# Kernel tuning notes

Measured on AMD Instinct MI355X. Metric: run time of the kernel, lower is better.

Reference implementation:

```python
import jax, jax.numpy as jnp
import numpy as np

N_TOKENS = 1024
HIDDEN = 2048
N_EXPERTS = 16
MOE_INTER = 1024
TOP_K = 6
N_GROUP = 4
TOPK_GROUP = 2
N_SHARED = 2
ROUTED_SCALING = 2.5
RENORM = True
CAPACITY = 1024  # >> N_TOKENS*TOP_K/N_EXPERTS = 384; overflow probability negligible


def setup_inputs() -> dict:
    key = jax.random.key(0)
    ks = jax.random.split(key, 7)
    s = 0.02
    return {
        'hidden_states': jax.random.normal(ks[0], (N_TOKENS, HIDDEN), jnp.float32),
        'gate_w': jax.random.normal(ks[1], (N_EXPERTS, HIDDEN), jnp.float32) * s,
        'gate_bias': jax.random.normal(ks[2], (N_EXPERTS,), jnp.float32) * s,
        'w_gate_up': jax.random.normal(ks[3], (N_EXPERTS, HIDDEN, 2 * MOE_INTER), jnp.float32) * s,
        'w_down': jax.random.normal(ks[4], (N_EXPERTS, MOE_INTER, HIDDEN), jnp.float32) * s,
        'shared_w_gate_up': jax.random.normal(ks[5], (HIDDEN, 2 * N_SHARED * MOE_INTER), jnp.float32) * s,
        'shared_w_down': jax.random.normal(ks[6], (N_SHARED * MOE_INTER, HIDDEN), jnp.float32) * s,
    }


def _swiglu(gu):
    # npu_swiglu with activate_left=True: silu(first half) * second half
    g, u = jnp.split(gu, 2, axis=-1)
    return jax.nn.silu(g) * u


def reference(hidden_states, gate_w, gate_bias, w_gate_up, w_down, shared_w_gate_up, shared_w_down):
    x = hidden_states
    N, H = x.shape
    E, K, C = N_EXPERTS, TOP_K, CAPACITY
    P = N * K  # number of (token, slot) pairs

    # ---- MoEGate: router logits + noaux_tc grouped top-k ----
    logits = x @ gate_w.T                              # [N, E]
    scores = jax.nn.sigmoid(logits)                    # sigmoid scoring (noaux_tc)
    s_corr = scores + gate_bias[None, :]
    sg = s_corr.reshape(N, N_GROUP, E // N_GROUP)
    group_scores = jax.lax.top_k(sg, 2)[0].sum(-1)     # top-2 sum per group [N, G]
    _, gidx = jax.lax.top_k(group_scores, TOPK_GROUP)
    gmask = jnp.sum(jax.nn.one_hot(gidx, N_GROUP, dtype=jnp.float32), axis=1) > 0
    masked = jnp.where(gmask[:, :, None], sg, -jnp.inf).reshape(N, E)
    _, topk_ids = jax.lax.top_k(masked, K)             # [N, K]
    w = jnp.take_along_axis(scores, topk_ids, axis=-1)  # weights from original scores
    if RENORM:
        w = w / jnp.sum(w, axis=-1, keepdims=True)
    w = w * ROUTED_SCALING

    # ---- dispatch: fixed-capacity buffers per expert ----
    flat_e = topk_ids.reshape(P)
    onehot = jax.nn.one_hot(flat_e, E, dtype=jnp.int32)
    pos = jnp.cumsum(onehot, axis=0)[jnp.arange(P), flat_e] - 1  # slot within expert
    valid = pos < C
    buf = jnp.full((E, C), P, jnp.int32).at[flat_e, jnp.clip(pos, 0, C - 1)].set(
        jnp.where(valid, jnp.arange(P, dtype=jnp.int32), P))
    tok = jnp.where(buf < P, buf // K, N)              # token index per slot, N = pad
    x_pad = jnp.concatenate([x, jnp.zeros((1, H), x.dtype)], axis=0)
    xe = x_pad[tok]                                    # [E, C, H]

    # ---- grouped expert GEMMs (SwiGLU MLP per expert) ----
    h = jnp.einsum('ech,ehi->eci', xe, w_gate_up)      # [E, C, 2I]
    y = jnp.einsum('eci,eih->ech', _swiglu(h), w_down)  # [E, C, H]

    # ---- combine: weighted scatter-add back to tokens ----
    w_pad = jnp.concatenate([w.reshape(P), jnp.zeros((1,), w.dtype)])
    pw = w_pad[jnp.where(buf < P, buf, P)]             # [E, C]
    routed = jnp.zeros((N + 1, H), x.dtype).at[tok].add(y * pw[:, :, None])[:N]

    # ---- shared experts (reduce_results=False, fused add) ----
    shared = _swiglu(x @ shared_w_gate_up) @ shared_w_down
    return routed + shared
```

## Files before the change

### kernel.cpp

```cpp
#include <hip/hip_runtime.h>
#include <hip/hip_bf16.h>
#include <math.h>

typedef __attribute__((ext_vector_type(8))) short bf16x8;
typedef __attribute__((ext_vector_type(4))) float f32x4;

#define N_TOK 1024
#define HID   2048
#define NEXP  16
#define NE2   18
#define INTER 1024
#define TOPK  6
#define CAP   1024

__device__ __forceinline__ unsigned short f2bf(float f) {
  unsigned u = __builtin_bit_cast(unsigned, f);
  u += 0x7fffu + ((u >> 16) & 1u);
  return (unsigned short)(u >> 16);
}
__device__ __forceinline__ float b2f(short s) {
  unsigned u = ((unsigned)(unsigned short)s) << 16;
  return __builtin_bit_cast(float, u);
}
__device__ __forceinline__ void gll16(const void* g, void* l) {
  __builtin_amdgcn_global_load_lds(
      (const __attribute__((address_space(1))) unsigned int*)g,
      (__attribute__((address_space(3))) unsigned int*)l, 16, 0, 0);
}

__global__ __launch_bounds__(256) void router_k(
    const float* __restrict__ x, const float* __restrict__ gw,
    const float* __restrict__ gb, int* __restrict__ counts,
    int* __restrict__ tok_list, int* __restrict__ meta,
    float* __restrict__ pwt, unsigned short* __restrict__ x_bf)
{
  const int t   = blockIdx.x;
  const int tid = threadIdx.x;
  __shared__ float xrow[HID];
  __shared__ float logits[NEXP];

  for (int i = tid; i < HID; i += 256) {
    float v = x[(size_t)t * HID + i];
    xrow[i] = v;
    x_bf[(size_t)t * HID + i] = f2bf(v);
  }
  __syncthreads();

  const int w = tid >> 6, lane = tid & 63;
  for (int s = 0; s < 4; ++s) {
    int e = w * 4 + s;
    const float* g = gw + (size_t)e * HID;
    float p = 0.f;
    for (int i = lane; i < HID; i += 64) p += xrow[i] * g[i];
    for (int off = 32; off; off >>= 1) p += __shfl_down(p, off);
    if (lane == 0) logits[e] = p;
  }
  __syncthreads();

  if (tid == 0) {
    float sc[NEXP], scorr[NEXP];
    for (int e = 0; e < NEXP; ++e) {
      float s1 = 1.f / (1.f + expf(-logits[e]));
      sc[e] = s1; scorr[e] = s1 + gb[e];
    }
    float gs[4];
    for (int g = 0; g < 4; ++g) {
      float m1 = -1e30f, m2 = -1e30f;
      for (int j = 0; j < 4; ++j) {
        float v = scorr[g * 4 + j];
        if (v > m1) { m2 = m1; m1 = v; } else if (v > m2) m2 = v;
      }
      gs[g] = m1 + m2;
    }
    int g1 = 0;
    for (int g = 1; g < 4; ++g) if (gs[g] > gs[g1]) g1 = g;
    int g2 = -1;
    for (int g = 0; g < 4; ++g) { if (g == g1) continue; if (g2 < 0 || gs[g] > gs[g2]) g2 = g; }

    bool taken[NEXP];
    for (int e = 0; e < NEXP; ++e) taken[e] = false;
    int ids[TOPK]; float wv[TOPK]; float wsum = 0.f;
    for (int k = 0; k < TOPK; ++k) {
      int best = -1; float bv = -1e30f;
      for (int e = 0; e < NEXP; ++e) {
        int grp = e >> 2;
        if (grp != g1 && grp != g2) continue;
        if (taken[e]) continue;
        if (scorr[e] > bv) { bv = scorr[e]; best = e; }
      }
      taken[best] = true; ids[k] = best; wv[k] = sc[best]; wsum += sc[best];
    }
    float inv = 2.5f / wsum;
    for (int k = 0; k < TOPK; ++k) {
      int e = ids[k];
      int slot = atomicAdd(&counts[e], 1);
      tok_list[e * CAP + slot] = t;
      meta[t * TOPK + k] = (e << 16) | slot;
      pwt[t * TOPK + k] = wv[k] * inv;
    }
  }
}

__global__ __launch_bounds__(256) void t_gu_k(
    const float* __restrict__ wgu, const float* __restrict__ sgu,
    unsigned short* __restrict__ dst)
{
  const int z = blockIdx.z;
  const int n0 = blockIdx.x * 64, k0 = blockIdx.y * 64;
  const float* src; int ld; int cb;
  if (z < 16) { src = wgu + (size_t)z * HID * (2 * INTER); ld = 2 * INTER; cb = n0; }
  else { int j = z - 16; src = sgu; ld = 4096;
         cb = (n0 < 1024) ? j * 1024 + n0 : 1024 * j + 1024 + n0; }
  __shared__ __align__(16) unsigned short t2[64][72];
  const int tid = threadIdx.x;
  const int kb = tid >> 4, nb = tid & 15;
  unsigned short h[4][4];
  #pragma unroll
  for (int j = 0; j < 4; ++j) {
    float4 f = *(const float4*)(src + (size_t)(k0 + kb * 4 + j) * ld + cb + nb * 4);
    h[j][0] = f2bf(f.x); h[j][1] = f2bf(f.y); h[j][2] = f2bf(f.z); h[j][3] = f2bf(f.w);
  }
  #pragma unroll
  for (int i = 0; i < 4; ++i) {
    int rr = nb * 4 + i;
    unsigned lo  = h[0][i] | ((unsigned)h[1][i] << 16);
    unsigned hi2 = h[2][i] | ((unsigned)h[3][i] << 16);
    unsigned long long v = (unsigned long long)lo | ((unsigned long long)hi2 << 32);
    *(unsigned long long*)((char*)t2 + rr * 144 + ((kb * 8) ^ ((rr & 7) << 4))) = v;
  }
  __syncthreads();
  unsigned short* d = dst + (size_t)z * HID * (2 * INTER);
  #pragma unroll
  for (int i = 0; i < 2; ++i) {
    int c = tid + 256 * i;
    int nl = c >> 3, s = c & 7;
    uint4 v = *(const uint4*)((const char*)t2 + nl * 144 + ((s * 16) ^ ((nl & 7) << 4)));
    *(uint4*)(d + (size_t)(n0 + nl) * HID + k0 + s * 8) = v;
  }
}

__global__ __launch_bounds__(256) void t_d_k(
    const float* __restrict__ wd, const float* __restrict__ sd,
    unsigned short* __restrict__ dst)
{
  const int z = blockIdx.z;
  const int n0 = blockIdx.x * 64, k0 = blockIdx.y * 64;
  const float* src = (z < 16) ? wd + (size_t)z * INTER * HID
                              : sd + (size_t)(z - 16) * INTER * HID;
  __shared__ __align__(16) unsigned short t2[64][72];
  const int tid = threadIdx.x;
  const int kb = tid >> 4, nb = tid & 15;
  unsigned short h[4][4];
  #pragma unroll
  for (int j = 0; j < 4; ++j) {
    float4 f = *(const float4*)(src + (size_t)(k0 + kb * 4 + j) * HID + n0 + nb * 4);
    h[j][0] = f2bf(f.x); h[j][1] = f2bf(f.y); h[j][2] = f2bf(f.z); h[j][3] = f2bf(f.w);
  }
  #pragma unroll
  for (int i = 0; i < 4; ++i) {
    int rr = nb * 4 + i;
    unsigned lo  = h[0][i] | ((unsigned)h[1][i] << 16);
    unsigned hi2 = h[2][i] | ((unsigned)h[3][i] << 16);
    unsigned long long v = (unsigned long long)lo | ((unsigned long long)hi2 << 32);
    *(unsigned long long*)((char*)t2 + rr * 144 + ((kb * 8) ^ ((rr & 7) << 4))) = v;
  }
  __syncthreads();
  unsigned short* d = dst + (size_t)z * HID * INTER;
  #pragma unroll
  for (int i = 0; i < 2; ++i) {
    int c = tid + 256 * i;
    int nl = c >> 3, s = c & 7;
    uint4 v = *(const uint4*)((const char*)t2 + nl * 144 + ((s * 16) ^ ((nl & 7) << 4)));
    *(uint4*)(d + (size_t)(n0 + nl) * INTER + k0 + s * 8) = v;
  }
}

template<int MODE>
__global__ __launch_bounds__(256, 2) void gemm_bf16_k(
    const unsigned short* __restrict__ A, int lda, size_t a_estride,
    const unsigned short* __restrict__ Wt, int K, size_t w_estride,
    const int* __restrict__ counts, const int* __restrict__ tok_list,
    unsigned short* __restrict__ outb, int out_ld, size_t out_estride)
{
  const int e  = blockIdx.z;
  const int m0 = blockIdx.y * 128;
  const int M  = (e < 16) ? counts[e] : N_TOK;
  if (m0 >= M) return;
  const int n0 = blockIdx.x * (MODE == 0 ? 128 : 256);

  __shared__ __align__(16) unsigned short Al[128 * 64];
  __shared__ __align__(16) unsigned short Bl[2][256 * 64];

  const int tid = threadIdx.x, lane = tid & 63, wid = tid >> 6;
  const int wm = wid >> 1, wn = wid & 1, l15 = lane & 15, hi = lane >> 4;

  const unsigned short* Ap = A + (size_t)e * a_estride;
  const unsigned short* Wp = Wt + (size_t)e * w_estride;

  const int r0 = tid >> 3, s0 = tid & 7, sl = s0 ^ (r0 & 7);
  const unsigned short* asrc[4]; int aoff[4];
  #pragma unroll
  for (int i = 0; i < 4; ++i) {
    int r = r0 + 32 * i;
    int slot = m0 + r;
    int row;
    if (MODE == 0) row = (e < 16) ? ((slot < M) ? tok_list[e * CAP + slot] : 0) : slot;
    else           row = slot;
    asrc[i] = Ap + (size_t)row * lda + sl * 8;
    aoff[i] = (tid + 256 * i) * 16;
  }
  const unsigned short* bpg;
  const unsigned short* bpu;
  if (MODE == 0) {
    bpg = Wp + (size_t)(n0 + r0) * K + sl * 8;
    bpu = Wp + (size_t)(1024 + n0 + r0) * K + sl * 8;
  } else {
    bpg = Wp + (size_t)(n0 + r0) * K + sl * 8;
    bpu = bpg + (size_t)128 * K;
  }
  const size_t bstep = (size_t)32 * K;

  int bn[8];
  #pragma unroll
  for (int ni = 0; ni < 8; ++ni) {
    if (MODE == 0) bn[ni] = (ni < 4) ? (wn * 64 + ni * 16) : (128 + wn * 64 + (ni - 4) * 16);
    else           bn[ni] = wn * 128 + ni * 16;
  }

  f32x4 acc[4][8];
  #pragma unroll
  for (int a0 = 0; a0 < 4; ++a0)
    #pragma unroll
    for (int b0 = 0; b0 < 8; ++b0) acc[a0][b0] = (f32x4){0.f, 0.f, 0.f, 0.f};

  #define ISSUE_B(buf, kt)                                                  \
    _Pragma("unroll")                                                       \
    for (int i = 0; i < 4; ++i)                                             \
      gll16(bpg + bstep * i + (kt), (char*)(buf) + (tid + 256 * i) * 16);   \
    _Pragma("unroll")                                                       \
    for (int i = 0; i < 4; ++i)                                             \
      gll16(bpu + bstep * i + (kt), (char*)(buf) + (tid + 256 * (i + 4)) * 16);
  #define ISSUE_A(kt)                                                       \
    _Pragma("unroll")                                                       \
    for (int i = 0; i < 4; ++i) gll16(asrc[i] + (kt), (char*)Al + aoff[i]);
  #define COMPUTE(Bb)                                                       \
    _Pragma("unroll")                                                       \
    for (int kk = 0; kk < 64; kk += 32) {                                   \
      bf16x8 af[4], bv[8];                                                  \
      _Pragma("unroll")                                                     \
      for (int mi = 0; mi < 4; ++mi) {                                      \
        int r = wm * 64 + mi * 16 + l15;                                    \
        int off = (r * 128 + (kk + hi * 8) * 2) ^ ((r & 7) << 4);           \
        af[mi] = *(const bf16x8*)((const char*)Al + off);                   \
      }                                                                     \
      _Pragma("unroll")                                                     \
      for (int ni = 0; ni < 8; ++ni) {                                      \
        int r = bn[ni] + l15;                                               \
        int off = (r * 128 + (kk + hi * 8) * 2) ^ ((r & 7) << 4);           \
        bv[ni] = *(const bf16x8*)((const char*)(Bb) + off);                 \
      }                                                                     \
      _Pragma("unroll")                                                     \
      for (int mi = 0; mi < 4; ++mi)                                        \
        _Pragma("unroll")                                                   \
        for (int ni = 0; ni < 8; ++ni)                                      \
          acc[mi][ni] = __builtin_amdgcn_mfma_f32_16x16x32_bf16(            \
              af[mi], bv[ni], acc[mi][ni], 0, 0, 0);                        \
    }

  const int nt = K >> 6;
  ISSUE_B(Bl[0], 0)
  ISSUE_A(0)
  asm volatile("s_waitcnt vmcnt(0)" ::: "memory");
  __builtin_amdgcn_s_barrier();

  int p = 0;
  for (int t = 0; t < nt; ++t) {
    const bool pf = (t + 1 < nt);
    if (pf) { ISSUE_B(Bl[p ^ 1], (t + 1) << 6) }
    COMPUTE(Bl[p])
    __builtin_amdgcn_s_barrier();
    if (pf) {
      ISSUE_A((t + 1) << 6)
      asm volatile("s_waitcnt vmcnt(0)" ::: "memory");
      __builtin_amdgcn_s_barrier();
    }
    p ^= 1;
  }
  #undef ISSUE_B
  #undef ISSUE_A
  #undef COMPUTE

  const int rbase = hi * 4;
  if (MODE == 0) {
    #pragma unroll
    for (int mi = 0; mi < 4; ++mi)
      #pragma unroll
      for (int rr = 0; rr < 4; ++rr) {
        int slot = m0 + wm * 64 + mi * 16 + rbase + rr;
        if (slot >= M) continue;
        #pragma unroll
        for (int ni = 0; ni < 4; ++ni) {
          float g = acc[mi][ni][rr], u = acc[mi][ni + 4][rr];
          float sv = g / (1.f + expf(-g)) * u;
          int col = n0 + wn * 64 + ni * 16 + l15;
          outb[(size_t)e * out_estride + (size_t)slot * out_ld + col] = f2bf(sv);
        }
      }
  } else {
    #pragma unroll
    for (int mi = 0; mi < 4; ++mi)
      #pragma unroll
      for (int rr = 0; rr < 4; ++rr) {
        int slot = m0 + wm * 64 + mi * 16 + rbase + rr;
        if (slot >= M) continue;
        unsigned short* row = outb + (size_t)e * out_estride + (size_t)slot * out_ld;
        #pragma unroll
        for (int ni = 0; ni < 8; ++ni)
          row[n0 + bn[ni] + l15] = f2bf(acc[mi][ni][rr]);
      }
  }
}

__global__ __launch_bounds__(256) void combine_k(
    const unsigned short* __restrict__ ybuf, const int* __restrict__ meta,
    const float* __restrict__ pwt, float* __restrict__ out)
{
  const int t = blockIdx.x;
  const int c0 = threadIdx.x * 8;
  float acc[8];
  {
    bf16x8 v0 = *(const bf16x8*)(ybuf + ((size_t)16 * CAP + t) * HID + c0);
    bf16x8 v1 = *(const bf16x8*)(ybuf + ((size_t)17 * CAP + t) * HID + c0);
    #pragma unroll
    for (int j = 0; j < 8; ++j) acc[j] = b2f(v0[j]) + b2f(v1[j]);
  }
  #pragma unroll
  for (int k = 0; k < TOPK; ++k) {
    int m = meta[t * TOPK + k];
    float w = pwt[t * TOPK + k];
    int e = m >> 16, s = m & 0xffff;
    bf16x8 v = *(const bf16x8*)(ybuf + ((size_t)e * CAP + s) * HID + c0);
    #pragma unroll
    for (int j = 0; j < 8; ++j) acc[j] += w * b2f(v[j]);
  }
  float4* o = (float4*)(out + (size_t)t * HID + c0);
  o[0] = make_float4(acc[0], acc[1], acc[2], acc[3]);
  o[1] = make_float4(acc[4], acc[5], acc[6], acc[7]);
}

extern "C" void kernel_launch(void* const* d_in, const int* in_sizes, int n_in,
                              void* d_out, int out_size, void* d_ws, size_t ws_size,
                              hipStream_t stream) {
  const float* x   = (const float*)d_in[0];
  const float* gw  = (const float*)d_in[1];
  const float* gb  = (const float*)d_in[2];
  const float* wgu = (const float*)d_in[3];
  const float* wd  = (const float*)d_in[4];
  const float* sgu = (const float*)d_in[5];
  const float* sd  = (const float*)d_in[6];
  float* out = (float*)d_out;

  char* ws = (char*)d_ws;
  int*   counts   = (int*)ws;
  int*   tok_list = (int*)(ws + 256);
  int*   meta     = (int*)(ws + 256 + 65536);
  float* pwt      = (float*)(ws + 256 + 65536 + 24576);
  unsigned short* x_bf  = (unsigned short*)(ws + 128 * 1024);
  unsigned short* act   = x_bf + (size_t)N_TOK * HID;
  unsigned short* ybuf  = act + (size_t)NE2 * CAP * INTER;
  unsigned short* wt_gu = ybuf + (size_t)NE2 * CAP * HID;
  unsigned short* wt_d  = wt_gu + (size_t)NE2 * HID * 2 * INTER;
  const size_t need = (size_t)((char*)(wt_d + (size_t)NE2 * HID * INTER) - ws);
  if (ws_size < need) return;

  hipMemsetAsync(counts, 0, 256, stream);
  router_k<<<N_TOK, 256, 0, stream>>>(x, gw, gb, counts, tok_list, meta, pwt, x_bf);

  t_gu_k<<<dim3(2 * INTER / 64, HID / 64, NE2), 256, 0, stream>>>(wgu, sgu, wt_gu);
  t_d_k<<<dim3(HID / 64, INTER / 64, NE2), 256, 0, stream>>>(wd, sd, wt_d);

  gemm_bf16_k<0><<<dim3(INTER / 128, CAP / 128, NE2), 256, 0, stream>>>(
      x_bf, HID, 0, wt_gu, HID, (size_t)HID * 2 * INTER, counts, tok_list,
      act, INTER, (size_t)CAP * INTER);
  gemm_bf16_k<1><<<dim3(HID / 256, CAP / 128, NE2), 256, 0, stream>>>(
      act, INTER, (size_t)CAP * INTER, wt_d, INTER, (size_t)HID * INTER, counts, nullptr,
      ybuf, HID, (size_t)CAP * HID);

  combine_k<<<N_TOK, 256, 0, stream>>>(ybuf, meta, pwt, out);
}
```

Before: 484.9 us.

## Shrink GEMM N-tile to 128x128 and double-buffer both A and B

The grouped expert GEMMs drop from a 128x256 output tile to a 128x128 tile, which halves the accumulators per thread and doubles the grid size. Both the A and B tiles are now double-buffered in LDS, so each k-step needs one issue/wait/barrier instead of two syncs with A loaded serially. The aim is better latency hiding and more blocks per CU (the launch-bounds min-blocks hint is removed). The cost is more re-reading of A across N tiles and more blocks overall.

```diff
diff --git a/kernel.cpp b/kernel.cpp
--- a/kernel.cpp
+++ b/kernel.cpp
@@ -176,7 +176,7 @@
 }
 
 template<int MODE>
-__global__ __launch_bounds__(256, 2) void gemm_bf16_k(
+__global__ __launch_bounds__(256) void gemm_bf16_k(
     const unsigned short* __restrict__ A, int lda, size_t a_estride,
     const unsigned short* __restrict__ Wt, int K, size_t w_estride,
     const int* __restrict__ counts, const int* __restrict__ tok_list,
@@ -186,10 +186,10 @@
   const int m0 = blockIdx.y * 128;
   const int M  = (e < 16) ? counts[e] : N_TOK;
   if (m0 >= M) return;
-  const int n0 = blockIdx.x * (MODE == 0 ? 128 : 256);
-
-  __shared__ __align__(16) unsigned short Al[128 * 64];
-  __shared__ __align__(16) unsigned short Bl[2][256 * 64];
+  const int n0 = blockIdx.x * (MODE == 0 ? 64 : 128);
+
+  __shared__ __align__(16) unsigned short Al[2][128 * 64];
+  __shared__ __align__(16) unsigned short Bl[2][128 * 64];
 
   const int tid = threadIdx.x, lane = tid & 63, wid = tid >> 6;
   const int wm = wid >> 1, wn = wid & 1, l15 = lane & 15, hi = lane >> 4;
@@ -197,97 +197,80 @@
   const unsigned short* Ap = A + (size_t)e * a_estride;
   const unsigned short* Wp = Wt + (size_t)e * w_estride;
 
-  const int r0 = tid >> 3, s0 = tid & 7, sl = s0 ^ (r0 & 7);
-  const unsigned short* asrc[4]; int aoff[4];
+  const unsigned short* asrc[4]; int soff[4];
+  const unsigned short* bsrc[4];
   #pragma unroll
   for (int i = 0; i < 4; ++i) {
-    int r = r0 + 32 * i;
+    int c = tid + 256 * i;
+    int r = c >> 3, s = c & 7, sl = s ^ (r & 7);
     int slot = m0 + r;
     int row;
     if (MODE == 0) row = (e < 16) ? ((slot < M) ? tok_list[e * CAP + slot] : 0) : slot;
     else           row = slot;
     asrc[i] = Ap + (size_t)row * lda + sl * 8;
-    aoff[i] = (tid + 256 * i) * 16;
-  }
-  const unsigned short* bpg;
-  const unsigned short* bpu;
-  if (MODE == 0) {
-    bpg = Wp + (size_t)(n0 + r0) * K + sl * 8;
-    bpu = Wp + (size_t)(1024 + n0 + r0) * K + sl * 8;
-  } else {
-    bpg = Wp + (size_t)(n0 + r0) * K + sl * 8;
-    bpu = bpg + (size_t)128 * K;
-  }
-  const size_t bstep = (size_t)32 * K;
-
-  int bn[8];
-  #pragma unroll
-  for (int ni = 0; ni < 8; ++ni) {
-    if (MODE == 0) bn[ni] = (ni < 4) ? (wn * 64 + ni * 16) : (128 + wn * 64 + (ni - 4) * 16);
-    else           bn[ni] = wn * 128 + ni * 16;
-  }
-
-  f32x4 acc[4][8];
+    soff[i] = c * 16;
+    int nrow = (MODE == 0) ? ((r < 64) ? n0 + r : 1024 + n0 + (r - 64)) : (n0 + r);
+    bsrc[i] = Wp + (size_t)nrow * K + sl * 8;
+  }
+
+  int bn[4];
+  if (MODE == 0) { bn[0] = wn*32; bn[1] = wn*32+16; bn[2] = 64+wn*32; bn[3] = 80+wn*32; }
+  else           { bn[0] = wn*64; bn[1] = wn*64+16; bn[2] = wn*64+32; bn[3] = wn*64+48; }
+
+  f32x4 acc[4][4];
   #pragma unroll
   for (int a0 = 0; a0 < 4; ++a0)
     #pragma unroll
-    for (int b0 = 0; b0 < 8; ++b0) acc[a0][b0] = (f32x4){0.f, 0.f, 0.f, 0.f};
-
-  #define ISSUE_B(buf, kt)                                                  \
+    for (int b0 = 0; b0 < 4; ++b0) acc[a0][b0] = (f32x4){0.f, 0.f, 0.f, 0.f};
+
+  #define ISSUE(buf_i, kt)                                                  \
     _Pragma("unroll")                                                       \
     for (int i = 0; i < 4; ++i)                                             \
-      gll16(bpg + bstep * i + (kt), (char*)(buf) + (tid + 256 * i) * 16);   \
+      gll16(bsrc[i] + (kt), (char*)Bl[buf_i] + soff[i]);                    \
     _Pragma("unroll")                                                       \
     for (int i = 0; i < 4; ++i)                                             \
-      gll16(bpu + bstep * i + (kt), (char*)(buf) + (tid + 256 * (i + 4)) * 16);
-  #define ISSUE_A(kt)                                                       \
-    _Pragma("unroll")                                                       \
-    for (int i = 0; i < 4; ++i) gll16(asrc[i] + (kt), (char*)Al + aoff[i]);
-  #define COMPUTE(Bb)                                                       \
+      gll16(asrc[i] + (kt), (char*)Al[buf_i] + soff[i]);
+  #define COMPUTE(buf_i)                                                    \
     _Pragma("unroll")                                                       \
     for (int kk = 0; kk < 64; kk += 32) {                                   \
-      bf16x8 af[4], bv[8];                                                  \
+      bf16x8 af[4], bv[4];                                                  \
       _Pragma("unroll")                                                     \
       for (int mi = 0; mi < 4; ++mi) {                                      \
         int r = wm * 64 + mi * 16 + l15;                                    \
         int off = (r * 128 + (kk + hi * 8) * 2) ^ ((r & 7) << 4);           \
-        af[mi] = *(const bf16x8*)((const char*)Al + off);                   \
+        af[mi] = *(const bf16x8*)((const char*)Al[buf_i] + off);            \
       }                                                                     \
       _Pragma("unroll")                                                     \
-      for (int ni = 0; ni < 8; ++ni) {                                      \
+      for (int ni = 0; ni < 4; ++ni) {                                      \
         int r = bn[ni] + l15;                                               \
         int off = (r * 128 + (kk + hi * 8) * 2) ^ ((r & 7) << 4);           \
-        bv[ni] = *(const bf16x8*)((const char*)(Bb) + off);                 \
+        bv[ni] = *(const bf16x8*)((const char*)Bl[buf_i] + off);            \
       }                                                                     \
       _Pragma("unroll")                                                     \
       for (int mi = 0; mi < 4; ++mi)                                        \
         _Pragma("unroll")                                                   \
-        for (int ni = 0; ni < 8; ++ni)                                      \
+        for (int ni = 0; ni < 4; ++ni)                                      \
           acc[mi][ni] = __builtin_amdgcn_mfma_f32_16x16x32_bf16(            \
               af[mi], bv[ni], acc[mi][ni], 0, 0, 0);                        \
     }
 
   const int nt = K >> 6;
-  ISSUE_B(Bl[0], 0)
-  ISSUE_A(0)
-  asm volatile("s_waitcnt vmcnt(0)" ::: "memory");
-  __builtin_amdgcn_s_barrier();
+  ISSUE(0, 0)
+  __syncthreads();
 
   int p = 0;
   for (int t = 0; t < nt; ++t) {
-    const bool pf = (t + 1 < nt);
-    if (pf) { ISSUE_B(Bl[p ^ 1], (t + 1) << 6) }
-    COMPUTE(Bl[p])
+    if (t + 1 < nt) {
+      const int kt1 = (t + 1) << 6;
+      if (p == 0) { ISSUE(1, kt1) } else { ISSUE(0, kt1) }
+    }
+    if (p == 0) { COMPUTE(0) } else { COMPUTE(1) }
+    asm volatile("s_waitcnt vmcnt(0)" ::: "memory");
+    asm volatile("s_waitcnt lgkmcnt(0)" ::: "memory");
     __builtin_amdgcn_s_barrier();
-    if (pf) {
-      ISSUE_A((t + 1) << 6)
-      asm volatile("s_waitcnt vmcnt(0)" ::: "memory");
-      __builtin_amdgcn_s_barrier();
-    }
     p ^= 1;
   }
-  #undef ISSUE_B
-  #undef ISSUE_A
+  #undef ISSUE
   #undef COMPUTE
 
   const int rbase = hi * 4;
@@ -299,10 +282,10 @@
         int slot = m0 + wm * 64 + mi * 16 + rbase + rr;
         if (slot >= M) continue;
         #pragma unroll
-        for (int ni = 0; ni < 4; ++ni) {
-          float g = acc[mi][ni][rr], u = acc[mi][ni + 4][rr];
+        for (int j = 0; j < 2; ++j) {
+          float g = acc[mi][j][rr], u = acc[mi][j + 2][rr];
           float sv = g / (1.f + expf(-g)) * u;
-          int col = n0 + wn * 64 + ni * 16 + l15;
+          int col = n0 + wn * 32 + j * 16 + l15;
           outb[(size_t)e * out_estride + (size_t)slot * out_ld + col] = f2bf(sv);
         }
       }
@@ -315,7 +298,7 @@
         if (slot >= M) continue;
         unsigned short* row = outb + (size_t)e * out_estride + (size_t)slot * out_ld;
         #pragma unroll
-        for (int ni = 0; ni < 8; ++ni)
+        for (int ni = 0; ni < 4; ++ni)
           row[n0 + bn[ni] + l15] = f2bf(acc[mi][ni][rr]);
       }
   }
@@ -379,10 +362,10 @@
   t_gu_k<<<dim3(2 * INTER / 64, HID / 64, NE2), 256, 0, stream>>>(wgu, sgu, wt_gu);
   t_d_k<<<dim3(HID / 64, INTER / 64, NE2), 256, 0, stream>>>(wd, sd, wt_d);
 
-  gemm_bf16_k<0><<<dim3(INTER / 128, CAP / 128, NE2), 256, 0, stream>>>(
+  gemm_bf16_k<0><<<dim3(INTER / 64, CAP / 128, NE2), 256, 0, stream>>>(
       x_bf, HID, 0, wt_gu, HID, (size_t)HID * 2 * INTER, counts, tok_list,
       act, INTER, (size_t)CAP * INTER);
-  gemm_bf16_k<1><<<dim3(HID / 256, CAP / 128, NE2), 256, 0, stream>>>(
+  gemm_bf16_k<1><<<dim3(HID / 128, CAP / 128, NE2), 256, 0, stream>>>(
       act, INTER, (size_t)CAP * INTER, wt_d, INTER, (size_t)HID * INTER, counts, nullptr,
       ybuf, HID, (size_t)CAP * HID);
 
```

Result: faster. 448.9 us (-7.4%).
